# Performance work log

Hardware: AMD Instinct MI355X
Metric: run time of the kernel (lower is better)

## Reference

```python
import jax, jax.numpy as jnp
import numpy as np

B, S, E, H, D = 4, 2048, 512, 8, 64
NEG = 1e13  # module uses -1e13, not -inf


def setup_inputs() -> dict:
    key = jax.random.key(0)
    ks = jax.random.split(key, 10)
    x = jax.random.normal(ks[0], (B, S, E), dtype=jnp.float32)
    padding_pos = jax.random.randint(ks[1], (B, S), 0, 2, dtype=jnp.int64)
    std = 0.01
    # weights stored [in, out]; torch Linear init: normal(0, 0.01) weights, default bias
    Wq = jax.random.normal(ks[2], (E, H * D), dtype=jnp.float32) * std
    Wk = jax.random.normal(ks[3], (E, H * D), dtype=jnp.float32) * std
    Wv = jax.random.normal(ks[4], (E, H * D), dtype=jnp.float32) * std
    Wo = jax.random.normal(ks[5], (H * D, E), dtype=jnp.float32) * std
    bq = jax.random.uniform(ks[6], (H * D,), dtype=jnp.float32, minval=-1, maxval=1) / np.sqrt(E)
    bk = jax.random.uniform(ks[7], (H * D,), dtype=jnp.float32, minval=-1, maxval=1) / np.sqrt(E)
    bv = jax.random.uniform(ks[8], (H * D,), dtype=jnp.float32, minval=-1, maxval=1) / np.sqrt(E)
    bo = jax.random.uniform(ks[9], (E,), dtype=jnp.float32, minval=-1, maxval=1) / np.sqrt(H * D)
    return {"x": x, "padding_pos": padding_pos, "Wq": Wq, "bq": bq, "Wk": Wk,
            "bk": bk, "Wv": Wv, "bv": bv, "Wo": Wo, "bo": bo}


def reference(x, padding_pos, Wq, bq, Wk, bk, Wv, bv, Wo, bo):
    b = x.shape[0]
    q = (x @ Wq + bq).reshape(b, S, H, D).transpose(0, 2, 1, 3)  # [B,H,S,D]
    k = (x @ Wk + bk).reshape(b, S, H, D).transpose(0, 2, 1, 3)
    v = (x @ Wv + bv).reshape(b, S, H, D).transpose(0, 2, 1, 3)
    att = jnp.einsum('bhqd,bhkd->bhqk', q, k) / jnp.sqrt(jnp.float32(D))
    pad = (padding_pos == 1)  # [B,S]
    # mask key columns and query rows (module masks both via broadcast fills)
    mask = pad[:, None, None, :] | pad[:, None, :, None]  # [B,1,S,S]
    att = jnp.where(mask, -NEG, att)
    att = jax.nn.softmax(att, axis=-1)
    out = jnp.einsum('bhqk,bhkd->bhqd', att, v)
    out = out.transpose(0, 2, 1, 3).reshape(b, S, H * D)
    return out @ Wo + bo
```

## Files before the change

kernel.cpp:

```cpp
#include <hip/hip_runtime.h>
#include <hip/hip_bf16.h>
#include <math.h>

#define Bb 4
#define Ss 2048
#define Ee 512
#define Hh 8
#define Dd 64
#define HD 512
#define Mm (Bb*Ss)
#define RPB 1536
#define QTMAX 24
#define AT 24

using bf16x8 = __attribute__((ext_vector_type(8))) short;
using f32x4  = __attribute__((ext_vector_type(4))) float;

typedef __attribute__((address_space(1))) const unsigned int gu32;
typedef __attribute__((address_space(3))) unsigned int lu32;
__device__ inline void glds16(const void* g, void* l) {
    __builtin_amdgcn_global_load_lds((gu32*)g, (lu32*)l, 16, 0, 0);
}

__device__ inline unsigned short f2bf(float f) {
    unsigned int u = __float_as_uint(f);
    unsigned int r = (u + 0x7fffu + ((u >> 16) & 1u)) >> 16;
    return (unsigned short)r;
}
__device__ inline float bf2f(unsigned short u) {
    return __uint_as_float((unsigned int)u << 16);
}
__device__ inline unsigned int cvtpk(float a, float b) {
    float2 t; t.x = a; t.y = b;
    union { __hip_bfloat162 h; unsigned int u; } z;
    z.h = __float22bfloat162_rn(t);
    return z.u;
}

__global__ __launch_bounds__(256) void prep(
    const int* __restrict__ pad,
    const float* __restrict__ Wq, const float* __restrict__ Wk,
    const float* __restrict__ Wv, const float* __restrict__ Wo,
    unsigned short* __restrict__ Wt,
    int* __restrict__ idx, int* __restrict__ rank, int* __restrict__ cnt)
{
    __shared__ float T[64][68];
    const int bi = blockIdx.x, tid = threadIdx.x;

    if (bi < 256) {
        const int w = bi >> 6;
        const float* W = (w == 0) ? Wq : (w == 1) ? Wk : (w == 2) ? Wv : Wo;
        const int tk0 = ((bi >> 3) & 7) * 64, tn0 = (bi & 7) * 64;
        #pragma unroll
        for (int l = 0; l < 4; ++l) {
            int fi = tid + l * 256;
            int r = fi >> 4, c4 = (fi & 15) * 4;
            *(float4*)&T[r][c4] = *(const float4*)(W + (size_t)(tk0 + r) * Ee + tn0 + c4);
        }
        __syncthreads();
        #pragma unroll
        for (int l = 0; l < 4; ++l) {
            int fi = tid + l * 256;
            int r2 = fi >> 4, c4 = (fi & 15) * 4;
            uint2 o;
            o.x = cvtpk(T[c4 + 0][r2], T[c4 + 1][r2]);
            o.y = cvtpk(T[c4 + 2][r2], T[c4 + 3][r2]);
            *(uint2*)(Wt + (size_t)w * 262144 + (size_t)(tn0 + r2) * Ee + tk0 + c4) = o;
        }
    } else {
        const int b = bi - 256;
        int* sc = (int*)&T[0][0];
        int loc[8], c = 0;
        #pragma unroll
        for (int j = 0; j < 8; ++j) {
            loc[j] = pad[b * Ss + tid * 8 + j];
            c += (loc[j] == 0);
        }
        sc[tid] = c;
        __syncthreads();
        for (int s = 1; s < 256; s <<= 1) {
            int v = (tid >= s) ? sc[tid - s] : 0;
            __syncthreads();
            sc[tid] += v;
            __syncthreads();
        }
        int off = sc[tid] - c;
        #pragma unroll
        for (int j = 0; j < 8; ++j)
            if (loc[j] == 0) {
                idx[b * Ss + off] = tid * 8 + j;
                rank[b * Ss + tid * 8 + j] = off;
                ++off;
            }
        if (tid == 255) cnt[b] = sc[255];
    }
}

__global__ __launch_bounds__(256) void gatherx(
    const float* __restrict__ x, const int* __restrict__ pad,
    const int* __restrict__ rank,
    unsigned short* __restrict__ xc, float* __restrict__ xpart)
{
    const int bx = blockIdx.x, tid = threadIdx.x;
    const int b = bx >> 4, i = bx & 15;
    const int c8 = (tid & 63) * 8, grp = tid >> 6;
    __shared__ float sm[4][512];

    float a8[8] = {};
    for (int it = 0; it < 32; ++it) {
        int s = i * 128 + grp * 32 + it;
        const float* pr = x + ((size_t)b * Ss + s) * Ee + c8;
        float4 f0 = *(const float4*)pr;
        float4 f1 = *(const float4*)(pr + 4);
        a8[0] += f0.x; a8[1] += f0.y; a8[2] += f0.z; a8[3] += f0.w;
        a8[4] += f1.x; a8[5] += f1.y; a8[6] += f1.z; a8[7] += f1.w;
        if (pad[b * Ss + s] == 0) {
            int rk = rank[b * Ss + s];
            uint4 v;
            v.x = cvtpk(f0.x, f0.y); v.y = cvtpk(f0.z, f0.w);
            v.z = cvtpk(f1.x, f1.y); v.w = cvtpk(f1.z, f1.w);
            *(uint4*)(xc + ((size_t)b * RPB + rk) * Ee + c8) = v;
        }
    }
    #pragma unroll
    for (int j = 0; j < 8; ++j) sm[grp][c8 + j] = a8[j];
    __syncthreads();
    int c0 = tid * 2;
    float s0 = sm[0][c0] + sm[1][c0] + sm[2][c0] + sm[3][c0];
    float s1 = sm[0][c0 + 1] + sm[1][c0 + 1] + sm[2][c0 + 1] + sm[3][c0 + 1];
    float2 o; o.x = s0; o.y = s1;
    *(float2*)(xpart + (size_t)(b * 16 + i) * Ee + c0) = o;
}

__global__ __launch_bounds__(256) void gemm_qkvt(
    const unsigned short* __restrict__ xc, const unsigned short* __restrict__ Wt,
    const float* __restrict__ bq, const float* __restrict__ bk, const float* __restrict__ bv,
    const int* __restrict__ cnt, const float* __restrict__ xpart,
    unsigned short* __restrict__ qo, unsigned short* __restrict__ ko,
    unsigned short* __restrict__ vt, float* __restrict__ vmw)
{
    const int z = blockIdx.z;
    const int bx = blockIdx.x;
    const int b = bx / 192, t = bx - b * 192;
    const int at = (z < 2) ? (t >> 3) : (t & 7);
    const int bt = (z < 2) ? (t & 7) : (t >> 3);
    const int cntb = cnt[b];
    const int tid = threadIdx.x, lane = tid & 63, wv = tid >> 6;
    const int quad = lane >> 4, l15 = lane & 15;
    const int wm = (wv >> 1) * 32, wn = (wv & 1) * 32;
    const int sw = (l15 >> 1) & 3;

    __shared__ unsigned short As0[64][32], Bs0[64][32];
    __shared__ unsigned short As1[64][32], Bs1[64][32];

    if (z == 2 && bt == AT - 1) {
        __shared__ float xm[512];
        for (int kk = tid; kk < 512; kk += 256) {
            float s = 0.f;
            #pragma unroll
            for (int p = 0; p < 16; ++p) s += xpart[(size_t)(b * 16 + p) * Ee + kk];
            xm[kk] = s;
        }
        __syncthreads();
        int col = at * 64 + (tid >> 2);
        int kh = (tid & 3) * 128;
        const unsigned short* wrow = Wt + (size_t)2 * 262144 + (size_t)col * Ee + kh;
        float s = 0.f;
        #pragma unroll 8
        for (int kk = 0; kk < 128; ++kk) s += xm[kh + kk] * bf2f(wrow[kk]);
        s += __shfl_xor(s, 1);
        s += __shfl_xor(s, 2);
        if ((tid & 3) == 0) vmw[(size_t)b * HD + col] = s * (1.0f / 2048.0f) + bv[col];
        return;
    }

    const int xcTile = (z < 2) ? at : bt;
    if (xcTile * 64 >= cntb) return;

    const unsigned short *Ap, *Bp;
    if (z < 2) {
        Ap = xc + ((size_t)b * RPB + at * 64) * Ee;
        Bp = Wt + (size_t)z * 262144 + (size_t)bt * 64 * Ee;
    } else {
        Ap = Wt + (size_t)2 * 262144 + (size_t)at * 64 * Ee;
        Bp = xc + ((size_t)b * RPB + bt * 64) * Ee;
    }

    f32x4 acc[2][2] = {};

    auto stage = [&](unsigned short (&A)[64][32], unsigned short (&B)[64][32], int k0) {
        int r = tid >> 2, c = tid & 3;
        int cg = (c ^ ((r >> 1) & 3)) * 8;
        glds16(Ap + (size_t)r * Ee + k0 + cg, &A[r][c * 8]);
        glds16(Bp + (size_t)r * Ee + k0 + cg, &B[r][c * 8]);
    };
    auto compute = [&](const unsigned short (&A)[64][32], const unsigned short (&B)[64][32]) {
        bf16x8 af[2], bfr[2];
        #pragma unroll
        for (int ms = 0; ms < 2; ++ms) af[ms] = *(const bf16x8*)&A[wm + ms * 16 + l15][(quad ^ sw) * 8];
        #pragma unroll
        for (int ns = 0; ns < 2; ++ns) bfr[ns] = *(const bf16x8*)&B[wn + ns * 16 + l15][(quad ^ sw) * 8];
        #pragma unroll
        for (int ms = 0; ms < 2; ++ms)
            #pragma unroll
            for (int ns = 0; ns < 2; ++ns)
                acc[ms][ns] = __builtin_amdgcn_mfma_f32_16x16x32_bf16(af[ms], bfr[ns], acc[ms][ns], 0, 0, 0);
    };

    stage(As0, Bs0, 0);
    for (int ki = 0; ki < 16; ki += 2) {
        __syncthreads();
        if (ki + 1 < 16) stage(As1, Bs1, (ki + 1) * 32);
        compute(As0, Bs0);
        __syncthreads();
        if (ki + 2 < 16) stage(As0, Bs0, (ki + 2) * 32);
        compute(As1, Bs1);
    }

    if (z < 2) {
        const float* bias = z ? bk : bq;
        unsigned short* dst = z ? ko : qo;
        #pragma unroll
        for (int ns = 0; ns < 2; ++ns) {
            int col = bt * 64 + wn + ns * 16 + l15;
            float bb = bias[col];
            #pragma unroll
            for (int ms = 0; ms < 2; ++ms) {
                #pragma unroll
                for (int r = 0; r < 4; ++r) {
                    int m = at * 64 + wm + ms * 16 + quad * 4 + r;
                    float val = acc[ms][ns][r] + bb;
                    if (z == 0) val *= 0.18033688f;
                    dst[((size_t)b * RPB + m) * HD + col] = f2bf(val);
                }
            }
        }
    } else {
        #pragma unroll
        for (int ms = 0; ms < 2; ++ms) {
            #pragma unroll
            for (int r = 0; r < 4; ++r) {
                int dg = at * 64 + wm + ms * 16 + quad * 4 + r;
                float bb = bv[dg];
                #pragma unroll
                for (int ns = 0; ns < 2; ++ns) {
                    int col = bt * 64 + wn + ns * 16 + l15;
                    vt[((size_t)b * HD + dg) * RPB + col] = f2bf(acc[ms][ns][r] + bb);
                }
            }
        }
    }
}

__global__ __launch_bounds__(256) void attn(
    const unsigned short* __restrict__ qc, const unsigned short* __restrict__ kc,
    const unsigned short* __restrict__ vtc, const int* __restrict__ cnt,
    unsigned short* __restrict__ pO, float* __restrict__ pL,
    const float* __restrict__ vmw, const unsigned short* __restrict__ Wt,
    const float* __restrict__ bo, float* __restrict__ opad)
{
    __shared__ unsigned short Ks[2][64][32], Vs[2][64][32];
    __shared__ float Ps[4][16][68];

    const int tid = threadIdx.x, wv = tid >> 6, lane = tid & 63;
    const int quad = lane >> 4, l15 = lane & 15;
    const int bh = blockIdx.x, b = bh >> 3, h = bh & 7;
    const int qt = blockIdx.y, half = blockIdx.z;
    const int sw = (l15 >> 1) & 3;

    if (qt >= QTMAX) {
        if (half || bh >= 8) return;
        const int b2 = bh >> 1, seg = bh & 1;
        float* vm = &Ps[0][0][0];
        for (int t = tid; t < 512; t += 256) vm[t] = vmw[(size_t)b2 * HD + t];
        __syncthreads();
        int cc = seg * 256 + tid;
        const unsigned short* wrow = Wt + (size_t)3 * 262144 + (size_t)cc * HD;
        float s = 0.f;
        #pragma unroll 8
        for (int k = 0; k < 512; ++k) s += vm[k] * bf2f(wrow[k]);
        opad[(size_t)b2 * Ee + cc] = s + bo[cc];
        return;
    }

    const int cntb = cnt[b];
    if (qt * 64 >= cntb) return;

    const int tot = (cntb + 63) >> 6;
    const int hsplit = (tot + 1) >> 1;
    const int kstart = half ? hsplit : 0;
    const int kend = half ? tot : hsplit;

    const unsigned short* qrow = qc + ((size_t)b * RPB + qt * 64 + wv * 16 + l15) * HD + h * Dd;
    bf16x8 aq0 = *(const bf16x8*)(qrow + quad * 8);
    bf16x8 aq1 = *(const bf16x8*)(qrow + 32 + quad * 8);

    const unsigned short* kcb = kc + (size_t)b * RPB * HD + h * Dd;
    const unsigned short* vtb = vtc + ((size_t)b * HD + h * Dd) * RPB;

    float li[4] = {};
    f32x4 oacc[4] = {};

    for (int kt = kstart; kt < kend; ++kt) {
        const int k0 = kt * 64;
        __syncthreads();
        #pragma unroll
        for (int l = 0; l < 2; ++l) {
            int ci = tid + l * 256;
            int s = ci >> 8, row = (ci >> 2) & 63, c = ci & 3;
            int cg = (c ^ ((row >> 1) & 3)) * 8;
            glds16(kcb + (size_t)(k0 + row) * HD + s * 32 + cg, &Ks[s][row][c * 8]);
            glds16(vtb + (size_t)row * RPB + k0 + s * 32 + cg, &Vs[s][row][c * 8]);
        }
        __syncthreads();

        f32x4 sa[4];
        #pragma unroll
        for (int nt = 0; nt < 4; ++nt) {
            bf16x8 k0f = *(const bf16x8*)&Ks[0][nt * 16 + l15][(quad ^ sw) * 8];
            bf16x8 k1f = *(const bf16x8*)&Ks[1][nt * 16 + l15][(quad ^ sw) * 8];
            f32x4 zz = {0.f, 0.f, 0.f, 0.f};
            zz = __builtin_amdgcn_mfma_f32_16x16x32_bf16(aq0, k0f, zz, 0, 0, 0);
            zz = __builtin_amdgcn_mfma_f32_16x16x32_bf16(aq1, k1f, zz, 0, 0, 0);
            sa[nt] = zz;
        }

        if (kt == tot - 1 && (cntb & 63)) {
            #pragma unroll
            for (int nt = 0; nt < 4; ++nt) {
                bool bad = (k0 + nt * 16 + l15) >= cntb;
                #pragma unroll
                for (int r = 0; r < 4; ++r)
                    if (bad) sa[nt][r] = -1e30f;
            }
        }

        #pragma unroll
        for (int nt = 0; nt < 4; ++nt)
            #pragma unroll
            for (int r = 0; r < 4; ++r) {
                float p = exp2f(sa[nt][r]);
                sa[nt][r] = p;
                li[r] += p;
            }

        #pragma unroll
        for (int r = 0; r < 4; ++r) {
            int qr = quad * 4 + r;
            #pragma unroll
            for (int nt = 0; nt < 4; ++nt)
                Ps[wv][qr][nt * 16 + l15] = sa[nt][r];
        }
        float4 p0 = *(const float4*)&Ps[wv][l15][quad * 8];
        float4 p1 = *(const float4*)&Ps[wv][l15][quad * 8 + 4];
        float4 p2 = *(const float4*)&Ps[wv][l15][32 + quad * 8];
        float4 p3 = *(const float4*)&Ps[wv][l15][32 + quad * 8 + 4];
        union U8 { unsigned int u[4]; bf16x8 v8; };
        U8 ap0, ap1;
        ap0.u[0] = cvtpk(p0.x, p0.y); ap0.u[1] = cvtpk(p0.z, p0.w);
        ap0.u[2] = cvtpk(p1.x, p1.y); ap0.u[3] = cvtpk(p1.z, p1.w);
        ap1.u[0] = cvtpk(p2.x, p2.y); ap1.u[1] = cvtpk(p2.z, p2.w);
        ap1.u[2] = cvtpk(p3.x, p3.y); ap1.u[3] = cvtpk(p3.z, p3.w);

        #pragma unroll
        for (int nt = 0; nt < 4; ++nt) {
            bf16x8 v0f = *(const bf16x8*)&Vs[0][nt * 16 + l15][(quad ^ sw) * 8];
            bf16x8 v1f = *(const bf16x8*)&Vs[1][nt * 16 + l15][(quad ^ sw) * 8];
            oacc[nt] = __builtin_amdgcn_mfma_f32_16x16x32_bf16(ap0.v8, v0f, oacc[nt], 0, 0, 0);
            oacc[nt] = __builtin_amdgcn_mfma_f32_16x16x32_bf16(ap1.v8, v1f, oacc[nt], 0, 0, 0);
        }
    }

    const size_t pbase = (((size_t)bh * QTMAX + qt) * 2 + half) * 4096;
    const size_t lbase = (((size_t)bh * QTMAX + qt) * 2 + half) * 64;
    #pragma unroll
    for (int r = 0; r < 4; ++r) {
        float ls = li[r];
        ls += __shfl_xor(ls, 1);
        ls += __shfl_xor(ls, 2);
        ls += __shfl_xor(ls, 4);
        ls += __shfl_xor(ls, 8);
        int prow = wv * 16 + quad * 4 + r;
        if (l15 == 0) pL[lbase + prow] = ls;
        #pragma unroll
        for (int nt = 0; nt < 4; ++nt)
            pO[pbase + (size_t)prow * 64 + nt * 16 + l15] = f2bf(oacc[nt][r]);
    }
}

__global__ __launch_bounds__(256) void combine(
    const unsigned short* __restrict__ pO, const float* __restrict__ pL,
    const int* __restrict__ cnt, unsigned short* __restrict__ aoc)
{
    const int bh = blockIdx.x, b = bh >> 3, h = bh & 7;
    const int qt = blockIdx.y, tid = threadIdx.x;
    const int cntb = cnt[b];
    if (qt * 64 >= cntb) return;
    const int row = tid >> 2, dch = (tid & 3) * 16;
    const int jq = qt * 64 + row;
    if (jq >= cntb) return;
    const size_t lb = ((size_t)bh * QTMAX + qt) * 2 * 64;
    float lsum = pL[lb + row] + pL[lb + 64 + row];
    float inv = (lsum > 0.f) ? 1.0f / lsum : 0.f;
    const size_t pb = ((size_t)bh * QTMAX + qt) * 2 * 4096 + (size_t)row * 64 + dch;
    union { uint4 q; unsigned short u[8]; } a0, a1, b0, b1;
    a0.q = *(const uint4*)(pO + pb);
    a1.q = *(const uint4*)(pO + pb + 8);
    b0.q = *(const uint4*)(pO + pb + 4096);
    b1.q = *(const uint4*)(pO + pb + 4096 + 8);
    uint4 o0, o1;
    float v0, v1;
    v0 = (bf2f(a0.u[0]) + bf2f(b0.u[0])) * inv; v1 = (bf2f(a0.u[1]) + bf2f(b0.u[1])) * inv;
    o0.x = cvtpk(v0, v1);
    v0 = (bf2f(a0.u[2]) + bf2f(b0.u[2])) * inv; v1 = (bf2f(a0.u[3]) + bf2f(b0.u[3])) * inv;
    o0.y = cvtpk(v0, v1);
    v0 = (bf2f(a0.u[4]) + bf2f(b0.u[4])) * inv; v1 = (bf2f(a0.u[5]) + bf2f(b0.u[5])) * inv;
    o0.z = cvtpk(v0, v1);
    v0 = (bf2f(a0.u[6]) + bf2f(b0.u[6])) * inv; v1 = (bf2f(a0.u[7]) + bf2f(b0.u[7])) * inv;
    o0.w = cvtpk(v0, v1);
    v0 = (bf2f(a1.u[0]) + bf2f(b1.u[0])) * inv; v1 = (bf2f(a1.u[1]) + bf2f(b1.u[1])) * inv;
    o1.x = cvtpk(v0, v1);
    v0 = (bf2f(a1.u[2]) + bf2f(b1.u[2])) * inv; v1 = (bf2f(a1.u[3]) + bf2f(b1.u[3])) * inv;
    o1.y = cvtpk(v0, v1);
    v0 = (bf2f(a1.u[4]) + bf2f(b1.u[4])) * inv; v1 = (bf2f(a1.u[5]) + bf2f(b1.u[5])) * inv;
    o1.z = cvtpk(v0, v1);
    v0 = (bf2f(a1.u[6]) + bf2f(b1.u[6])) * inv; v1 = (bf2f(a1.u[7]) + bf2f(b1.u[7])) * inv;
    o1.w = cvtpk(v0, v1);
    unsigned short* dst = aoc + ((size_t)b * RPB + jq) * HD + h * Dd + dch;
    *(uint4*)dst = o0;
    *(uint4*)(dst + 8) = o1;
}

__global__ __launch_bounds__(256) void gemm_out(
    const unsigned short* __restrict__ a_in, const unsigned short* __restrict__ Wt,
    const float* __restrict__ bo, const int* __restrict__ idx,
    const int* __restrict__ cnt, const int* __restrict__ pad,
    const float* __restrict__ out_pad, float* __restrict__ out)
{
    const int bx = blockIdx.x;
    const int tid = threadIdx.x;

    if (bx >= Bb * 192) {
        const int fb = bx - Bb * 192;
        const int b = fb >> 3, seg = fb & 7;
        const int c0 = tid * 2;
        float2 op = *(const float2*)(out_pad + (size_t)b * Ee + c0);
        for (int r = 0; r < 256; ++r) {
            int s = seg * 256 + r;
            if (pad[b * Ss + s])
                *(float2*)(out + ((size_t)b * Ss + s) * Ee + c0) = op;
        }
        return;
    }

    const int b = bx / 192, t = bx - b * 192;
    const int at = t >> 3, bt = t & 7;
    const int cntb = cnt[b];
    if (at * 64 >= cntb) return;

    const unsigned short* Wz = Wt + (size_t)3 * 262144;
    const int lane = tid & 63, wv = tid >> 6;
    const int quad = lane >> 4, l15 = lane & 15;
    const int wm = (wv >> 1) * 32, wn = (wv & 1) * 32;
    const int sw = (l15 >> 1) & 3;
    const unsigned short* Ab = a_in + ((size_t)b * RPB + at * 64) * HD;
    const unsigned short* Bp = Wz + (size_t)bt * 64 * HD;

    __shared__ unsigned short As0[64][32], Bs0[64][32];
    __shared__ unsigned short As1[64][32], Bs1[64][32];

    f32x4 acc[2][2] = {};

    auto stage = [&](unsigned short (&A)[64][32], unsigned short (&B)[64][32], int k0) {
        int r = tid >> 2, c = tid & 3;
        int cg = (c ^ ((r >> 1) & 3)) * 8;
        glds16(Ab + (size_t)r * HD + k0 + cg, &A[r][c * 8]);
        glds16(Bp + (size_t)r * HD + k0 + cg, &B[r][c * 8]);
    };
    auto compute = [&](const unsigned short (&A)[64][32], const unsigned short (&B)[64][32]) {
        bf16x8 af[2], bfr[2];
        #pragma unroll
        for (int ms = 0; ms < 2; ++ms) af[ms] = *(const bf16x8*)&A[wm + ms * 16 + l15][(quad ^ sw) * 8];
        #pragma unroll
        for (int ns = 0; ns < 2; ++ns) bfr[ns] = *(const bf16x8*)&B[wn + ns * 16 + l15][(quad ^ sw) * 8];
        #pragma unroll
        for (int ms = 0; ms < 2; ++ms)
            #pragma unroll
            for (int ns = 0; ns < 2; ++ns)
                acc[ms][ns] = __builtin_amdgcn_mfma_f32_16x16x32_bf16(af[ms], bfr[ns], acc[ms][ns], 0, 0, 0);
    };

    stage(As0, Bs0, 0);
    for (int ki = 0; ki < 16; ki += 2) {
        __syncthreads();
        if (ki + 1 < 16) stage(As1, Bs1, (ki + 1) * 32);
        compute(As0, Bs0);
        __syncthreads();
        if (ki + 2 < 16) stage(As0, Bs0, (ki + 2) * 32);
        compute(As1, Bs1);
    }

    #pragma unroll
    for (int ns = 0; ns < 2; ++ns) {
        int col = bt * 64 + wn + ns * 16 + l15;
        float bb = bo[col];
        #pragma unroll
        for (int ms = 0; ms < 2; ++ms) {
            #pragma unroll
            for (int r = 0; r < 4; ++r) {
                int m = at * 64 + wm + ms * 16 + quad * 4 + r;
                if (m < cntb) {
                    int srow = idx[b * Ss + m];
                    out[((size_t)b * Ss + srow) * Ee + col] = acc[ms][ns][r] + bb;
                }
            }
        }
    }
}

extern "C" void kernel_launch(void* const* d_in, const int* in_sizes, int n_in,
                              void* d_out, int out_size, void* d_ws, size_t ws_size,
                              hipStream_t stream) {
    const float* x   = (const float*)d_in[0];
    const int*   pad = (const int*)  d_in[1];
    const float* Wq  = (const float*)d_in[2];
    const float* bq  = (const float*)d_in[3];
    const float* Wk  = (const float*)d_in[4];
    const float* bk  = (const float*)d_in[5];
    const float* Wv  = (const float*)d_in[6];
    const float* bv  = (const float*)d_in[7];
    const float* Wo  = (const float*)d_in[8];
    const float* bo  = (const float*)d_in[9];
    float* out = (float*)d_out;

    const size_t csz = (size_t)Bb * RPB * HD;
    unsigned short* Wt  = (unsigned short*)d_ws;
    unsigned short* qc  = Wt + 1048576;
    unsigned short* kc  = qc + csz;
    unsigned short* vtc = kc + csz;
    unsigned short* aoc = vtc + csz;
    unsigned short* xc  = aoc + csz;
    unsigned short* pO  = xc;
    unsigned short* tail = xc + 6291456;
    float* xpart = (float*)tail;
    int*   idxw  = (int*)(xpart + 64 * 512);
    int*   rankw = idxw + Mm;
    int*   cntw  = rankw + Mm;
    float* vmw   = (float*)(cntw + 4);
    float* opad  = vmw + Bb * HD;
    float* pLw   = opad + Bb * Ee;

    prep<<<260, 256, 0, stream>>>(pad, Wq, Wk, Wv, Wo, Wt, idxw, rankw, cntw);

    gatherx<<<64, 256, 0, stream>>>(x, pad, rankw, xc, xpart);

    dim3 g1(Bb * 192, 1, 3);
    gemm_qkvt<<<g1, 256, 0, stream>>>(xc, Wt, bq, bk, bv, cntw, xpart, qc, kc, vtc, vmw);

    dim3 g2(Bb * Hh, QTMAX + 1, 2);
    attn<<<g2, 256, 0, stream>>>(qc, kc, vtc, cntw, pO, pLw, vmw, Wt, bo, opad);

    dim3 g3(Bb * Hh, QTMAX);
    combine<<<g3, 256, 0, stream>>>(pO, pLw, cntw, aoc);

    dim3 g4(Bb * 192 + 32, 1);
    gemm_out<<<g4, 256, 0, stream>>>(aoc, Wt, bo, idxw, cntw, pad, opad, out);
}
```

Baseline: 165.8 us.

## Fuse gather into prep and fold split-K combine into output GEMM

Merges the pad-scan/weight-transpose kernel with the x gather/compaction kernel: each gather block redoes the per-batch prefix scan and keeps the row ranks in shared memory, so the global rank array and one launch go away. It also removes the combine kernel. The output GEMM now loads both partial attention outputs, normalises them by the summed softmax denominators and converts to bf16 while staging the A tile into LDS. This saves two launches and the aoc round trip through memory. In exchange the scan runs redundantly in 16 blocks per batch, and A staging becomes synchronous register loads instead of async global-to-LDS copies.

```diff
diff --git a/kernel.cpp b/kernel.cpp
--- a/kernel.cpp
+++ b/kernel.cpp
@@ -37,14 +37,17 @@
     return z.u;
 }
 
-__global__ __launch_bounds__(256) void prep(
-    const int* __restrict__ pad,
+__global__ __launch_bounds__(256) void prep2(
+    const float* __restrict__ x, const int* __restrict__ pad,
     const float* __restrict__ Wq, const float* __restrict__ Wk,
     const float* __restrict__ Wv, const float* __restrict__ Wo,
-    unsigned short* __restrict__ Wt,
-    int* __restrict__ idx, int* __restrict__ rank, int* __restrict__ cnt)
+    unsigned short* __restrict__ Wt, unsigned short* __restrict__ xc,
+    float* __restrict__ xpart, int* __restrict__ idx, int* __restrict__ cnt)
 {
-    __shared__ float T[64][68];
+    __shared__ union ShMem {
+        float T[64][68];
+        struct { int sc[256]; int rk[128]; float sm[4][512]; } g;
+    } sh;
     const int bi = blockIdx.x, tid = threadIdx.x;
 
     if (bi < 256) {
@@ -55,7 +58,7 @@
         for (int l = 0; l < 4; ++l) {
             int fi = tid + l * 256;
             int r = fi >> 4, c4 = (fi & 15) * 4;
-            *(float4*)&T[r][c4] = *(const float4*)(W + (size_t)(tk0 + r) * Ee + tn0 + c4);
+            *(float4*)&sh.T[r][c4] = *(const float4*)(W + (size_t)(tk0 + r) * Ee + tn0 + c4);
         }
         __syncthreads();
         #pragma unroll
@@ -63,71 +66,69 @@
             int fi = tid + l * 256;
             int r2 = fi >> 4, c4 = (fi & 15) * 4;
             uint2 o;
-            o.x = cvtpk(T[c4 + 0][r2], T[c4 + 1][r2]);
-            o.y = cvtpk(T[c4 + 2][r2], T[c4 + 3][r2]);
+            o.x = cvtpk(sh.T[c4 + 0][r2], sh.T[c4 + 1][r2]);
+            o.y = cvtpk(sh.T[c4 + 2][r2], sh.T[c4 + 3][r2]);
             *(uint2*)(Wt + (size_t)w * 262144 + (size_t)(tn0 + r2) * Ee + tk0 + c4) = o;
         }
-    } else {
-        const int b = bi - 256;
-        int* sc = (int*)&T[0][0];
-        int loc[8], c = 0;
+        return;
+    }
+
+    const int gb = bi - 256;
+    const int b = gb >> 4, i = gb & 15;
+
+    int loc[8], c = 0;
+    #pragma unroll
+    for (int j = 0; j < 8; ++j) {
+        loc[j] = pad[b * Ss + tid * 8 + j];
+        c += (loc[j] == 0);
+    }
+    sh.g.sc[tid] = c;
+    __syncthreads();
+    for (int s = 1; s < 256; s <<= 1) {
+        int v = (tid >= s) ? sh.g.sc[tid - s] : 0;
+        __syncthreads();
+        sh.g.sc[tid] += v;
+        __syncthreads();
+    }
+    if (tid >= i * 16 && tid < i * 16 + 16) {
+        int off = sh.g.sc[tid] - c;
+        int lbase = (tid - i * 16) * 8;
         #pragma unroll
         for (int j = 0; j < 8; ++j) {
-            loc[j] = pad[b * Ss + tid * 8 + j];
-            c += (loc[j] == 0);
-        }
-        sc[tid] = c;
-        __syncthreads();
-        for (int s = 1; s < 256; s <<= 1) {
-            int v = (tid >= s) ? sc[tid - s] : 0;
-            __syncthreads();
-            sc[tid] += v;
-            __syncthreads();
-        }
-        int off = sc[tid] - c;
-        #pragma unroll
-        for (int j = 0; j < 8; ++j)
             if (loc[j] == 0) {
                 idx[b * Ss + off] = tid * 8 + j;
-                rank[b * Ss + tid * 8 + j] = off;
+                sh.g.rk[lbase + j] = off;
                 ++off;
-            }
-        if (tid == 255) cnt[b] = sc[255];
-    }
-}
-
-__global__ __launch_bounds__(256) void gatherx(
-    const float* __restrict__ x, const int* __restrict__ pad,
-    const int* __restrict__ rank,
-    unsigned short* __restrict__ xc, float* __restrict__ xpart)
-{
-    const int bx = blockIdx.x, tid = threadIdx.x;
-    const int b = bx >> 4, i = bx & 15;
+            } else sh.g.rk[lbase + j] = -1;
+        }
+    }
+    if (i == 15 && tid == 255) cnt[b] = sh.g.sc[255];
+    __syncthreads();
+
     const int c8 = (tid & 63) * 8, grp = tid >> 6;
-    __shared__ float sm[4][512];
-
     float a8[8] = {};
     for (int it = 0; it < 32; ++it) {
-        int s = i * 128 + grp * 32 + it;
+        int lr = grp * 32 + it;
+        int s = i * 128 + lr;
         const float* pr = x + ((size_t)b * Ss + s) * Ee + c8;
         float4 f0 = *(const float4*)pr;
         float4 f1 = *(const float4*)(pr + 4);
         a8[0] += f0.x; a8[1] += f0.y; a8[2] += f0.z; a8[3] += f0.w;
         a8[4] += f1.x; a8[5] += f1.y; a8[6] += f1.z; a8[7] += f1.w;
-        if (pad[b * Ss + s] == 0) {
-            int rk = rank[b * Ss + s];
+        int rkk = sh.g.rk[lr];
+        if (rkk >= 0) {
             uint4 v;
             v.x = cvtpk(f0.x, f0.y); v.y = cvtpk(f0.z, f0.w);
             v.z = cvtpk(f1.x, f1.y); v.w = cvtpk(f1.z, f1.w);
-            *(uint4*)(xc + ((size_t)b * RPB + rk) * Ee + c8) = v;
+            *(uint4*)(xc + ((size_t)b * RPB + rkk) * Ee + c8) = v;
         }
     }
     #pragma unroll
-    for (int j = 0; j < 8; ++j) sm[grp][c8 + j] = a8[j];
+    for (int j = 0; j < 8; ++j) sh.g.sm[grp][c8 + j] = a8[j];
     __syncthreads();
     int c0 = tid * 2;
-    float s0 = sm[0][c0] + sm[1][c0] + sm[2][c0] + sm[3][c0];
-    float s1 = sm[0][c0 + 1] + sm[1][c0 + 1] + sm[2][c0 + 1] + sm[3][c0 + 1];
+    float s0 = sh.g.sm[0][c0] + sh.g.sm[1][c0] + sh.g.sm[2][c0] + sh.g.sm[3][c0];
+    float s1 = sh.g.sm[0][c0 + 1] + sh.g.sm[1][c0 + 1] + sh.g.sm[2][c0 + 1] + sh.g.sm[3][c0 + 1];
     float2 o; o.x = s0; o.y = s1;
     *(float2*)(xpart + (size_t)(b * 16 + i) * Ee + c0) = o;
 }
@@ -388,54 +389,12 @@
     }
 }
 
-__global__ __launch_bounds__(256) void combine(
+__global__ __launch_bounds__(256) void gemm_out(
     const unsigned short* __restrict__ pO, const float* __restrict__ pL,
-    const int* __restrict__ cnt, unsigned short* __restrict__ aoc)
-{
-    const int bh = blockIdx.x, b = bh >> 3, h = bh & 7;
-    const int qt = blockIdx.y, tid = threadIdx.x;
-    const int cntb = cnt[b];
-    if (qt * 64 >= cntb) return;
-    const int row = tid >> 2, dch = (tid & 3) * 16;
-    const int jq = qt * 64 + row;
-    if (jq >= cntb) return;
-    const size_t lb = ((size_t)bh * QTMAX + qt) * 2 * 64;
-    float lsum = pL[lb + row] + pL[lb + 64 + row];
-    float inv = (lsum > 0.f) ? 1.0f / lsum : 0.f;
-    const size_t pb = ((size_t)bh * QTMAX + qt) * 2 * 4096 + (size_t)row * 64 + dch;
-    union { uint4 q; unsigned short u[8]; } a0, a1, b0, b1;
-    a0.q = *(const uint4*)(pO + pb);
-    a1.q = *(const uint4*)(pO + pb + 8);
-    b0.q = *(const uint4*)(pO + pb + 4096);
-    b1.q = *(const uint4*)(pO + pb + 4096 + 8);
-    uint4 o0, o1;
-    float v0, v1;
-    v0 = (bf2f(a0.u[0]) + bf2f(b0.u[0])) * inv; v1 = (bf2f(a0.u[1]) + bf2f(b0.u[1])) * inv;
-    o0.x = cvtpk(v0, v1);
-    v0 = (bf2f(a0.u[2]) + bf2f(b0.u[2])) * inv; v1 = (bf2f(a0.u[3]) + bf2f(b0.u[3])) * inv;
-    o0.y = cvtpk(v0, v1);
-    v0 = (bf2f(a0.u[4]) + bf2f(b0.u[4])) * inv; v1 = (bf2f(a0.u[5]) + bf2f(b0.u[5])) * inv;
-    o0.z = cvtpk(v0, v1);
-    v0 = (bf2f(a0.u[6]) + bf2f(b0.u[6])) * inv; v1 = (bf2f(a0.u[7]) + bf2f(b0.u[7])) * inv;
-    o0.w = cvtpk(v0, v1);
-    v0 = (bf2f(a1.u[0]) + bf2f(b1.u[0])) * inv; v1 = (bf2f(a1.u[1]) + bf2f(b1.u[1])) * inv;
-    o1.x = cvtpk(v0, v1);
-    v0 = (bf2f(a1.u[2]) + bf2f(b1.u[2])) * inv; v1 = (bf2f(a1.u[3]) + bf2f(b1.u[3])) * inv;
-    o1.y = cvtpk(v0, v1);
-    v0 = (bf2f(a1.u[4]) + bf2f(b1.u[4])) * inv; v1 = (bf2f(a1.u[5]) + bf2f(b1.u[5])) * inv;
-    o1.z = cvtpk(v0, v1);
-    v0 = (bf2f(a1.u[6]) + bf2f(b1.u[6])) * inv; v1 = (bf2f(a1.u[7]) + bf2f(b1.u[7])) * inv;
-    o1.w = cvtpk(v0, v1);
-    unsigned short* dst = aoc + ((size_t)b * RPB + jq) * HD + h * Dd + dch;
-    *(uint4*)dst = o0;
-    *(uint4*)(dst + 8) = o1;
-}
-
-__global__ __launch_bounds__(256) void gemm_out(
-    const unsigned short* __restrict__ a_in, const unsigned short* __restrict__ Wt,
-    const float* __restrict__ bo, const int* __restrict__ idx,
-    const int* __restrict__ cnt, const int* __restrict__ pad,
-    const float* __restrict__ out_pad, float* __restrict__ out)
+    const unsigned short* __restrict__ Wt, const float* __restrict__ bo,
+    const int* __restrict__ idx, const int* __restrict__ cnt,
+    const int* __restrict__ pad, const float* __restrict__ out_pad,
+    float* __restrict__ out)
 {
     const int bx = blockIdx.x;
     const int tid = threadIdx.x;
@@ -463,18 +422,44 @@
     const int quad = lane >> 4, l15 = lane & 15;
     const int wm = (wv >> 1) * 32, wn = (wv & 1) * 32;
     const int sw = (l15 >> 1) & 3;
-    const unsigned short* Ab = a_in + ((size_t)b * RPB + at * 64) * HD;
     const unsigned short* Bp = Wz + (size_t)bt * 64 * HD;
 
     __shared__ unsigned short As0[64][32], Bs0[64][32];
     __shared__ unsigned short As1[64][32], Bs1[64][32];
+    __shared__ float invSh[512];
+
+    #pragma unroll
+    for (int l = 0; l < 2; ++l) {
+        int ix = tid + l * 256;
+        int h = ix >> 6, row = ix & 63;
+        size_t lb = ((size_t)(b * 8 + h) * QTMAX + at) * 2 * 64;
+        float lsum = pL[lb + row] + pL[lb + 64 + row];
+        invSh[ix] = (lsum > 0.f) ? 1.0f / lsum : 0.f;
+    }
+    __syncthreads();
 
     f32x4 acc[2][2] = {};
 
-    auto stage = [&](unsigned short (&A)[64][32], unsigned short (&B)[64][32], int k0) {
+    auto stageA = [&](unsigned short (&A)[64][32], int k0) {
+        int r = tid >> 2, c = tid & 3;
+        int swr = (r >> 1) & 3;
+        int h = k0 >> 6;
+        int d0 = (k0 & 63) + c * 8;
+        const size_t pb = ((size_t)((b * 8 + h) * QTMAX + at) * 2) * 4096 + (size_t)r * 64 + d0;
+        union { uint4 q; unsigned short u[8]; } pa, pbh;
+        pa.q  = *(const uint4*)(pO + pb);
+        pbh.q = *(const uint4*)(pO + pb + 4096);
+        float inv = invSh[h * 64 + r];
+        uint4 o;
+        o.x = cvtpk((bf2f(pa.u[0]) + bf2f(pbh.u[0])) * inv, (bf2f(pa.u[1]) + bf2f(pbh.u[1])) * inv);
+        o.y = cvtpk((bf2f(pa.u[2]) + bf2f(pbh.u[2])) * inv, (bf2f(pa.u[3]) + bf2f(pbh.u[3])) * inv);
+        o.z = cvtpk((bf2f(pa.u[4]) + bf2f(pbh.u[4])) * inv, (bf2f(pa.u[5]) + bf2f(pbh.u[5])) * inv);
+        o.w = cvtpk((bf2f(pa.u[6]) + bf2f(pbh.u[6])) * inv, (bf2f(pa.u[7]) + bf2f(pbh.u[7])) * inv);
+        *(uint4*)&A[r][(c ^ swr) * 8] = o;
+    };
+    auto stageB = [&](unsigned short (&B)[64][32], int k0) {
         int r = tid >> 2, c = tid & 3;
         int cg = (c ^ ((r >> 1) & 3)) * 8;
-        glds16(Ab + (size_t)r * HD + k0 + cg, &A[r][c * 8]);
         glds16(Bp + (size_t)r * HD + k0 + cg, &B[r][c * 8]);
     };
     auto compute = [&](const unsigned short (&A)[64][32], const unsigned short (&B)[64][32]) {
@@ -490,13 +475,13 @@
                 acc[ms][ns] = __builtin_amdgcn_mfma_f32_16x16x32_bf16(af[ms], bfr[ns], acc[ms][ns], 0, 0, 0);
     };
 
-    stage(As0, Bs0, 0);
+    stageA(As0, 0); stageB(Bs0, 0);
     for (int ki = 0; ki < 16; ki += 2) {
         __syncthreads();
-        if (ki + 1 < 16) stage(As1, Bs1, (ki + 1) * 32);
+        if (ki + 1 < 16) { stageA(As1, (ki + 1) * 32); stageB(Bs1, (ki + 1) * 32); }
         compute(As0, Bs0);
         __syncthreads();
-        if (ki + 2 < 16) stage(As0, Bs0, (ki + 2) * 32);
+        if (ki + 2 < 16) { stageA(As0, (ki + 2) * 32); stageB(Bs0, (ki + 2) * 32); }
         compute(As1, Bs1);
     }
 
@@ -538,21 +523,17 @@
     unsigned short* qc  = Wt + 1048576;
     unsigned short* kc  = qc + csz;
     unsigned short* vtc = kc + csz;
-    unsigned short* aoc = vtc + csz;
-    unsigned short* xc  = aoc + csz;
+    unsigned short* xc  = vtc + csz;
     unsigned short* pO  = xc;
     unsigned short* tail = xc + 6291456;
     float* xpart = (float*)tail;
     int*   idxw  = (int*)(xpart + 64 * 512);
-    int*   rankw = idxw + Mm;
-    int*   cntw  = rankw + Mm;
+    int*   cntw  = idxw + Mm;
     float* vmw   = (float*)(cntw + 4);
     float* opad  = vmw + Bb * HD;
     float* pLw   = opad + Bb * Ee;
 
-    prep<<<260, 256, 0, stream>>>(pad, Wq, Wk, Wv, Wo, Wt, idxw, rankw, cntw);
-
-    gatherx<<<64, 256, 0, stream>>>(x, pad, rankw, xc, xpart);
+    prep2<<<320, 256, 0, stream>>>(x, pad, Wq, Wk, Wv, Wo, Wt, xc, xpart, idxw, cntw);
 
     dim3 g1(Bb * 192, 1, 3);
     gemm_qkvt<<<g1, 256, 0, stream>>>(xc, Wt, bq, bk, bv, cntw, xpart, qc, kc, vtc, vmw);
@@ -560,9 +541,6 @@
     dim3 g2(Bb * Hh, QTMAX + 1, 2);
     attn<<<g2, 256, 0, stream>>>(qc, kc, vtc, cntw, pO, pLw, vmw, Wt, bo, opad);
 
-    dim3 g3(Bb * Hh, QTMAX);
-    combine<<<g3, 256, 0, stream>>>(pO, pLw, cntw, aoc);
-
-    dim3 g4(Bb * 192 + 32, 1);
-    gemm_out<<<g4, 256, 0, stream>>>(aoc, Wt, bo, idxw, cntw, pad, opad, out);
-}
+    dim3 g3(Bb * 192 + 32, 1);
+    gemm_out<<<g3, 256, 0, stream>>>(pO, pLw, Wt, bo, idxw, cntw, pad, opad, out);
+}
```

Measured after the change: 164.2 us. No clear change (-0.9%).
